# Performance work log

Hardware: AMD Instinct MI355X
Metric: run time of the kernel (lower is better)

Reference implementation:

```python
import jax, jax.numpy as jnp
import numpy as np

B, D_IN, D_OUT, DICT = 2048, 768, 768, 24576
TOP_K, TOP_K_AUX = 32, 512
L1_COEFF, AUX_PENALTY, N_DEAD = 0.001, 0.03125, 100.0


def setup_inputs() -> dict:
    key = jax.random.key(0)
    k1, k2, k3, k4, k5, k6 = jax.random.split(key, 6)
    x_in = jax.random.normal(k1, (B, D_IN), dtype=jnp.float32)
    y_target = jax.random.normal(k2, (B, D_OUT), dtype=jnp.float32)
    nb = jax.random.randint(k3, (DICT,), 0, 200).astype(jnp.float32)
    # kaiming-uniform-ish init
    bound_e = float(np.sqrt(6.0 / D_IN))
    W_enc = jax.random.uniform(k4, (D_IN, DICT), minval=-bound_e, maxval=bound_e, dtype=jnp.float32)
    bound_d = float(np.sqrt(6.0 / DICT))
    W_dec = jax.random.uniform(k5, (DICT, D_OUT), minval=-bound_d, maxval=bound_d, dtype=jnp.float32)
    W_dec = W_dec / jnp.linalg.norm(W_dec, axis=-1, keepdims=True)  # unit-norm rows
    b_dec = jnp.zeros((D_OUT,), dtype=jnp.float32)
    return {"x_in": x_in, "y_target": y_target, "num_batches_not_active": nb,
            "W_enc": W_enc, "W_dec": W_dec, "b_dec": b_dec}


def _unit_norm(x):
    m = x.mean(axis=-1, keepdims=True)
    x = x - m
    s = jnp.std(x, axis=-1, keepdims=True, ddof=1)  # torch .std is unbiased
    return x / (s + 1e-5), m, s


def reference(x_in, y_target, num_batches_not_active, W_enc, W_dec, b_dec):
    xn, _, _ = _unit_norm(x_in)
    yn, y_mean, y_std = _unit_norm(y_target)
    x_enc = xn - b_dec  # pre_enc_bias (input_size == output_size)
    acts = jax.nn.relu(x_enc @ W_enc)                      # [B, DICT]
    vals, idx = jax.lax.top_k(acts, TOP_K)                 # [B, TOP_K]
    rows = jnp.arange(B)[:, None]
    acts_sparse = jnp.zeros_like(acts).at[rows, idx].set(vals)
    y_pred = acts_sparse @ W_dec + b_dec                   # [B, D_OUT]
    y_pred_out = y_pred * y_std + y_mean

    # stateful dead-feature bookkeeping (update_inactive_features)
    col_active = acts_sparse.sum(axis=0) > 0
    nb = jnp.where(col_active, 0.0, num_batches_not_active + 1.0)

    l2_loss = jnp.mean((y_pred - yn) ** 2)
    l1_norm = jnp.mean(jnp.abs(acts_sparse).sum(axis=-1))
    l1_loss = L1_COEFF * l1_norm
    l0_norm = jnp.mean((acts_sparse > 0).astype(jnp.float32).sum(axis=-1))

    # auxiliary loss on dead features (static-shape masked top-k; masked cols
    # get -1 < relu acts so extras relu-clip to 0 -> same math as torch gather)
    dead = nb >= N_DEAD
    masked = jnp.where(dead[None, :], acts, -1.0)
    av, ai = jax.lax.top_k(masked, TOP_K_AUX)
    av = jax.nn.relu(av)
    acts_aux = jnp.zeros_like(acts).at[rows, ai].set(av)
    y_pred_aux = acts_aux @ W_dec
    residual = yn - y_pred
    l2_aux = AUX_PENALTY * jnp.mean((y_pred_aux - residual) ** 2)
    aux_loss = jnp.where(dead.any(), l2_aux, 0.0)

    loss = l2_loss + l1_loss + aux_loss
    num_dead_features = (nb > N_DEAD).sum()
    return (y_pred_out, acts_sparse, loss, l2_loss, l1_loss, l0_norm, l1_norm,
            aux_loss, num_dead_features)
```

## Files before the change

### kernel.cpp

```cpp
#include <hip/hip_runtime.h>
#include <math.h>

#define BATCH 2048
#define DIN 768
#define DICT 24576
#define KM 32
#define KA 512
#define NPT 48
#define L1_COEFF 0.001f
#define AUX_PENALTY 0.03125f
#define CAND_MAX 128
#define CAND_DELTA 0.08f
#define AUX_SPLIT 8
#define SAUX 18432
#define AGB ((DIN/128)*(BATCH/128)*AUX_SPLIT)

typedef __attribute__((ext_vector_type(8))) short bf16x8;
typedef __attribute__((ext_vector_type(8))) unsigned short u16x8;
typedef __attribute__((ext_vector_type(4))) float f32x4;

constexpr size_t WS_XENC   = 0;
constexpr size_t WS_YN     = WS_XENC + (size_t)BATCH*DIN;
constexpr size_t WS_YMEAN  = WS_YN + (size_t)BATCH*DIN;
constexpr size_t WS_YSTD   = WS_YMEAN + BATCH;
constexpr size_t WS_RES    = WS_YSTD + BATCH;
constexpr size_t WS_NSEL   = WS_RES + (size_t)BATCH*DIN;
constexpr size_t WS_SEL    = WS_NSEL + BATCH;
constexpr size_t WS_SELV   = WS_SEL + (size_t)BATCH*KM;
constexpr size_t WS_COLACT = WS_SELV + (size_t)BATCH*KM;
constexpr size_t WS_ACC    = WS_COLACT + DICT;
constexpr size_t WS_DB     = WS_ACC + 8;
constexpr size_t WS_XEB    = WS_DB + DICT/32;
constexpr size_t WS_WETF   = WS_XEB + (size_t)BATCH*DIN/2;
constexpr size_t WS_WETB   = WS_WETF + (size_t)DICT*DIN;
constexpr size_t WS_WDB    = WS_WETB + (size_t)DICT*DIN/2;
constexpr size_t WS_DPREF  = WS_XEB + DICT/32;
constexpr size_t WS_META   = WS_XEB + 2*(DICT/32);

__device__ __forceinline__ unsigned short f2b(float f){
    unsigned u = __float_as_uint(f);
    return (unsigned short)((u + 0x7fffu + ((u >> 16) & 1u)) >> 16);
}
__device__ __forceinline__ float b2f(unsigned short h){ return __uint_as_float(((unsigned)h) << 16); }

__device__ __forceinline__ void gld_lds16(const void* g, void* l){
    __builtin_amdgcn_global_load_lds(
        (const __attribute__((address_space(1))) unsigned int*)g,
        (__attribute__((address_space(3))) unsigned int*)l, 16, 0, 0);
}

__device__ __forceinline__ int blk_count512_w(int cw, int* s16, int par){
    if ((threadIdx.x & 63) == 0) s16[par*8 + (threadIdx.x >> 6)] = cw;
    __syncthreads();
    int tot = 0;
    #pragma unroll
    for (int w=0; w<8; w++) tot += s16[par*8+w];
    return tot;
}
__device__ __forceinline__ float blk_sum512(float v, float* s16, int par){
    #pragma unroll
    for (int off=32; off; off>>=1) v += __shfl_down(v, off);
    if ((threadIdx.x & 63) == 0) s16[par*8 + (threadIdx.x >> 6)] = v;
    __syncthreads();
    float t = 0.f;
    #pragma unroll
    for (int w=0; w<8; w++) t += s16[par*8+w];
    return t;
}
__device__ __forceinline__ float blk_sum256(float v, float* s8, int par){
    #pragma unroll
    for (int off=32; off; off>>=1) v += __shfl_down(v, off);
    if ((threadIdx.x & 63) == 0) s8[par*4 + (threadIdx.x >> 6)] = v;
    __syncthreads();
    float t = 0.f;
    #pragma unroll
    for (int w=0; w<4; w++) t += s8[par*4+w];
    return t;
}

__global__ __launch_bounds__(256) void prep_k(const float* __restrict__ x,
        const float* __restrict__ y, const float* __restrict__ bdec,
        const float* __restrict__ We, const float* __restrict__ Wd,
        float* __restrict__ Tf, unsigned short* __restrict__ Tb,
        unsigned short* __restrict__ Td, float* __restrict__ ws){
    __shared__ float s8[8];
    __shared__ float t1[32][33];
    __shared__ float t2[32][33];
    const int tid = threadIdx.x;
    if (blockIdx.x < 2*BATCH){
        int b = blockIdx.x; bool isy = b >= BATCH; int row = isy ? b - BATCH : b;
        if (b < 8){
            float* dst = ws + WS_COLACT;
            for (int i = b*256 + tid; i < DICT + 8; i += 2048) dst[i] = 0.f;
        }
        const float* src = (isy ? y : x) + (size_t)row*DIN;
        float v0 = src[tid], v1 = src[tid+256], v2 = src[tid+512];
        float s = blk_sum256(v0+v1+v2, s8, 0);
        float mean = s * (1.f/(float)DIN);
        float d0 = v0-mean, d1 = v1-mean, d2 = v2-mean;
        float vs = blk_sum256(d0*d0+d1*d1+d2*d2, s8, 1);
        float sd = sqrtf(vs / (float)(DIN-1));
        float inv = 1.f / (sd + 1e-5f);
        if (isy){
            float* yn = ws + WS_YN + (size_t)row*DIN;
            yn[tid] = d0*inv; yn[tid+256] = d1*inv; yn[tid+512] = d2*inv;
            if (tid==0){ ws[WS_YMEAN+row] = mean; ws[WS_YSTD+row] = sd; }
        } else {
            float* xe = ws + WS_XENC + (size_t)row*DIN;
            unsigned short* xeb = (unsigned short*)(ws + WS_XEB) + (size_t)row*DIN;
            float e0 = d0*inv - bdec[tid];
            float e1 = d1*inv - bdec[tid+256];
            float e2 = d2*inv - bdec[tid+512];
            xe[tid] = e0; xe[tid+256] = e1; xe[tid+512] = e2;
            xeb[tid] = f2b(e0); xeb[tid+256] = f2b(e1); xeb[tid+512] = f2b(e2);
        }
    } else {
        int t = blockIdx.x - 2*BATCH;
        int bx = t % (DICT/32), by = t / (DICT/32);
        int a0 = bx*32, k0 = by*32;
        int r = tid >> 5, c = tid & 31;
        #pragma unroll
        for (int rr=r; rr<32; rr+=8){
            t1[rr][c] = We[(size_t)(k0+rr)*DICT + a0 + c];
            t2[rr][c] = Wd[(size_t)(a0+rr)*DIN + k0 + c];
        }
        __syncthreads();
        #pragma unroll
        for (int rr=r; rr<32; rr+=8){
            float v = t1[c][rr];
            Tf[(size_t)(a0+rr)*DIN + k0 + c] = v;
            Tb[(size_t)(a0+rr)*DIN + k0 + c] = f2b(v);
            Td[(size_t)(k0+rr)*DICT + a0 + c] = f2b(t2[c][rr]);
        }
    }
}

__global__ __launch_bounds__(256) void gemm_mfma(const unsigned short* __restrict__ Abf,
        const unsigned short* __restrict__ Bbf, unsigned short* __restrict__ C){
    __shared__ __align__(16) unsigned short As[128*64];
    __shared__ __align__(16) unsigned short Bs[128*64];
    const int tid = threadIdx.x;
    const int w = tid >> 6, lane = tid & 63;
    const int g = blockIdx.x;
    const int xcd = g & 7;
    const int s_ = g >> 3;
    const int m_t = s_ & 15;
    const int n_t = xcd + 8*(s_ >> 4);
    const int m0 = m_t*128, n0 = n_t*128;
    const int srow = lane >> 3;
    const int schunk = (lane & 7) ^ srow;
    const int wm = (w >> 1)*64, wn = (w & 1)*64;
    f32x4 acc[16];
    #pragma unroll
    for (int i=0;i<16;i++) acc[i] = (f32x4){0.f,0.f,0.f,0.f};
    for (int kt = 0; kt < DIN; kt += 64){
        #pragma unroll
        for (int q=0;q<4;q++){
            int s = w*4 + q;
            int row = 8*s + srow;
            gld_lds16(Abf + (size_t)(m0+row)*DIN + kt + schunk*8, &As[8*s*64]);
            gld_lds16(Bbf + (size_t)(n0+row)*DIN + kt + schunk*8, &Bs[8*s*64]);
        }
        __syncthreads();
        #pragma unroll
        for (int kk=0; kk<64; kk+=32){
            bf16x8 af[4], bfr[4];
            int ch = (kk>>3) + (lane>>4);
            #pragma unroll
            for (int i=0;i<4;i++){
                int row = wm + i*16 + (lane&15);
                af[i] = *(const bf16x8*)&As[row*64 + ((ch ^ (row&7))<<3)];
            }
            #pragma unroll
            for (int j=0;j<4;j++){
                int row = wn + j*16 + (lane&15);
                bfr[j] = *(const bf16x8*)&Bs[row*64 + ((ch ^ (row&7))<<3)];
            }
            #pragma unroll
            for (int i=0;i<4;i++)
                #pragma unroll
                for (int j=0;j<4;j++)
                    acc[i*4+j] = __builtin_amdgcn_mfma_f32_16x16x32_bf16(af[i], bfr[j], acc[i*4+j], 0,0,0);
        }
        __syncthreads();
    }
    #pragma unroll
    for (int i=0;i<4;i++){
        #pragma unroll
        for (int r=0;r<4;r++){
            int m = m0 + wm + i*16 + (lane>>4)*4 + r;
            unsigned short* crow = C + (size_t)m*DICT + n0 + wn + (lane&15);
            #pragma unroll
            for (int j=0;j<4;j++)
                crow[j*16] = f2b(fmaxf(acc[i*4+j][r], 0.f) + 0.0f);
        }
    }
}

__global__ __launch_bounds__(512) void topk_main(const unsigned short* __restrict__ actsb,
        const float* __restrict__ WeTf, const float* __restrict__ Wdec,
        const float* __restrict__ bdec, float* __restrict__ ws,
        float* __restrict__ ypred_out){
    const int row = blockIdx.x, tid = threadIdx.x;
    const int lane = tid & 63, wid = tid >> 6;
    __shared__ int   s_i16[16];
    __shared__ float s_f16[16];
    __shared__ float s_x[DIN];
    __shared__ int   s_ci[CAND_MAX];
    __shared__ float s_cv[CAND_MAX];
    __shared__ int   s_li[KM];
    __shared__ float s_lv[KM];
    __shared__ int   s_n, s_m;
    const unsigned short* arow = actsb + (size_t)row * DICT;
    const float* xrow = ws + WS_XENC + (size_t)row * DIN;
    unsigned short h[NPT];
    #pragma unroll
    for (int i=0;i<6;i++){
        u16x8 v = *(const u16x8*)&arow[i*4096 + tid*8];
        #pragma unroll
        for (int e=0;e<8;e++) h[i*8+e] = v[e];
    }
    s_x[tid] = xrow[tid];
    if (tid < DIN-512) s_x[tid+512] = xrow[tid+512];
    if (tid == 0){ s_n = 0; s_m = 0; }

    int par = 0;
    unsigned prefix = 0;
    for (int bit=14; bit>=0; bit--){
        unsigned cand = prefix | (1u<<bit);
        int c = 0;
        #pragma unroll
        for (int q=0;q<NPT;q++) c += (int)__popcll(__ballot((unsigned)h[q] >= cand));
        int tot = blk_count512_w(c, s_i16, par); par ^= 1;
        if (tot >= KM) prefix = cand;
    }
    float tc = b2f((unsigned short)prefix) - CAND_DELTA;
    #pragma unroll
    for (int q=0;q<NPT;q++){
        if (b2f(h[q]) > tc){
            int p = atomicAdd(&s_n, 1);
            if (p < CAND_MAX) s_ci[p] = (q>>3)*4096 + tid*8 + (q&7);
        }
    }
    __syncthreads();
    int nc = s_n; if (nc > CAND_MAX) nc = CAND_MAX;
    for (int c = wid; c < nc; c += 8){
        const float* wr = WeTf + (size_t)s_ci[c]*DIN;
        float p = 0.f;
        #pragma unroll
        for (int t=0; t<12; t++) p = fmaf(s_x[lane + 64*t], wr[lane + 64*t], p);
        #pragma unroll
        for (int off=32; off; off>>=1) p += __shfl_down(p, off);
        if (lane == 0) s_cv[c] = fmaxf(p, 0.f);
    }
    __syncthreads();
    if (tid < nc){
        float vi = s_cv[tid]; int ii = s_ci[tid];
        int rank = 0;
        for (int j=0; j<nc; j++){
            float vj = s_cv[j];
            rank += (vj > vi) || (vj == vi && s_ci[j] < ii);
        }
        if (rank < KM){
            int p = atomicAdd(&s_m, 1);
            s_li[p] = ii; s_lv[p] = vi;
        }
    }
    __syncthreads();
    if (tid < KM){
        ((int*)ws)[WS_COLACT + s_li[tid]] = 1;
        ((int*)ws)[WS_SEL  + (size_t)row*KM + tid] = s_li[tid];
        ws[WS_SELV + (size_t)row*KM + tid] = s_lv[tid];
    }
    if (tid == 0){
        float l1 = 0.f; int l0 = 0;
        for (int l=0;l<KM;l++){ l1 += s_lv[l]; l0 += (s_lv[l] > 0.f); }
        atomicAdd(&ws[WS_ACC+1], l1);
        atomicAdd(&ws[WS_ACC+2], (float)l0);
    }
    __syncthreads();
    float ym = ws[WS_YMEAN+row], ys = ws[WS_YSTD+row];
    float l2loc = 0.f;
    for (int c = tid; c < DIN; c += 512){
        float acc = bdec[c];
        #pragma unroll 4
        for (int l=0;l<KM;l++) acc = fmaf(s_lv[l], Wdec[(size_t)s_li[l]*DIN + c], acc);
        float ynv = ws[WS_YN + (size_t)row*DIN + c];
        float d = acc - ynv;
        l2loc += d*d;
        ws[WS_RES + (size_t)row*DIN + c] = ynv - acc;
        ypred_out[(size_t)row*DIN + c] = fmaf(acc, ys, ym);
    }
    float l2t = blk_sum512(l2loc, s_f16, 0);
    if (tid==0) atomicAdd(&ws[WS_ACC+0], l2t);
}

__global__ __launch_bounds__(768) void deadscan_k(const float* __restrict__ nb,
        float* __restrict__ ws){
    __shared__ int s[DICT/32];
    __shared__ int c12[12];
    const int t = threadIdx.x;
    const int* colact = (const int*)ws + WS_COLACT;
    unsigned bits = 0; int cgt = 0;
    const int base = t*32;
    #pragma unroll 8
    for (int b=0;b<32;b++){
        int j = base + b;
        float nbn = colact[j] ? 0.f : nb[j] + 1.f;
        bits |= (nbn >= 100.f ? 1u : 0u) << b;
        cgt  += (nbn > 100.f) ? 1 : 0;
    }
    ((unsigned*)(ws + WS_DB))[t] = bits;
    int pc = __popc(bits);
    s[t] = pc;
    #pragma unroll
    for (int off=32; off; off>>=1) cgt += __shfl_down(cgt, off);
    if ((t & 63) == 0) c12[t >> 6] = cgt;
    __syncthreads();
    for (int off=1; off<DICT/32; off<<=1){
        int v = (t >= off) ? s[t-off] : 0;
        __syncthreads();
        s[t] += v;
        __syncthreads();
    }
    ((int*)(ws + WS_DPREF))[t] = s[t] - pc;
    if (t == DICT/32 - 1){
        int nd = s[t];
        int ndpad = (nd + 63) & ~63;
        if (ndpad > SAUX) ndpad = SAUX;
        int* meta = (int*)(ws + WS_META);
        meta[0] = nd; meta[1] = ndpad; meta[2] = ndpad >> 6;
        meta[3] = ((ndpad >> 6) + AUX_SPLIT - 1) / AUX_SPLIT;
        int tot = 0;
        #pragma unroll
        for (int wv=0; wv<12; wv++) tot += c12[wv];
        ws[WS_ACC+4] = (float)tot;
        ((int*)ws)[WS_ACC+5] = (nd > 0) ? 1 : 0;
    }
}

__global__ __launch_bounds__(512) void auxprep_k(const unsigned short* __restrict__ actsb,
        unsigned short* __restrict__ wdt, unsigned short* __restrict__ auxc,
        float* __restrict__ ws){
    __shared__ unsigned s_db[DICT/32];
    __shared__ int      s_dp[DICT/32];
    __shared__ int      s_i16[16];
    __shared__ unsigned short s_out[SAUX];
    const int tid = threadIdx.x;
    for (int i=tid; i<DICT/32; i+=512){
        s_db[i] = ((const unsigned*)(ws + WS_DB))[i];
        s_dp[i] = ((const int*)(ws + WS_DPREF))[i];
    }
    const int nd    = ((const int*)(ws + WS_META))[0];
    const int ndpad = ((const int*)(ws + WS_META))[1];
    __syncthreads();
    if (blockIdx.x < DIN){
        const int n = blockIdx.x;
        unsigned short* row = wdt + (size_t)n*DICT;
        #pragma unroll
        for (int i=0;i<6;i++){
            u16x8 a = *(const u16x8*)&row[i*4096 + tid*8];
            int w = i*128 + (tid>>2);
            unsigned dbw = s_db[w]; int dpw = s_dp[w];
            #pragma unroll
            for (int e=0;e<8;e++){
                int bit = (tid&3)*8 + e;
                if ((dbw >> bit) & 1u){
                    int p = dpw + __popc(dbw & ((1u<<bit)-1u));
                    if (p < SAUX) s_out[p] = a[e];
                }
            }
        }
        for (int t2 = nd + tid; t2 < ndpad; t2 += 512) s_out[t2] = 0;
        __syncthreads();
        for (int i = tid*8; i < ndpad; i += 4096)
            *(u16x8*)&row[i] = *(const u16x8*)&s_out[i];
    } else {
        const int row = blockIdx.x - DIN;
        const unsigned short* arow = actsb + (size_t)row * DICT;
        unsigned short key[NPT];
        #pragma unroll
        for (int i=0;i<6;i++){
            u16x8 v = *(const u16x8*)&arow[i*4096 + tid*8];
            unsigned dbw = s_db[i*128 + (tid>>2)];
            #pragma unroll
            for (int e=0;e<8;e++){
                unsigned short hv = v[e];
                key[i*8+e] = (((dbw >> ((tid&3)*8 + e)) & 1u) && hv) ? hv : 0;
            }
        }
        int par = 0;
        unsigned prefix = 0;
        for (int bit=14; bit>=0; bit--){
            unsigned cand = prefix | (1u<<bit);
            int c = 0;
            #pragma unroll
            for (int q=0;q<NPT;q++) c += (int)__popcll(__ballot((unsigned)key[q] >= cand));
            int tot = blk_count512_w(c, s_i16, par); par ^= 1;
            if (tot >= KA) prefix = cand;
        }
        unsigned thr = prefix ? prefix : 1u;
        #pragma unroll
        for (int i=0;i<6;i++){
            int w = i*128 + (tid>>2);
            unsigned dbw = s_db[w];
            int dpw = s_dp[w];
            #pragma unroll
            for (int e=0;e<8;e++){
                int bit = (tid&3)*8 + e;
                if ((dbw >> bit) & 1u){
                    int p = dpw + __popc(dbw & ((1u<<bit)-1u));
                    unsigned short kv = key[i*8+e];
                    if (p < SAUX) s_out[p] = ((unsigned)kv >= thr) ? kv : (unsigned short)0;
                }
            }
        }
        for (int t2 = nd + tid; t2 < ndpad; t2 += 512) s_out[t2] = 0;
        __syncthreads();
        unsigned short* crow = auxc + (size_t)row * SAUX;
        for (int i = tid*8; i < ndpad; i += 4096)
            *(u16x8*)&crow[i] = *(const u16x8*)&s_out[i];
    }
}

__global__ __launch_bounds__(256) void auxgz_k(const unsigned short* __restrict__ Abf,
        const unsigned short* __restrict__ Bbf, float* __restrict__ ws,
        float* __restrict__ acts){
    __shared__ __align__(16) unsigned short As[128*64];
    __shared__ __align__(16) unsigned short Bs[128*64];
    const int tid = threadIdx.x;
    if (blockIdx.x >= AGB){
        const int row = blockIdx.x - AGB;
        float4 z = make_float4(0.f,0.f,0.f,0.f);
        float4* arow4 = (float4*)(acts + (size_t)row*DICT);
        #pragma unroll
        for (int i=0;i<24;i++) arow4[tid + 256*i] = z;
        __syncthreads();
        if (tid < KM){
            int j   = ((const int*)ws)[WS_SEL + (size_t)row*KM + tid];
            float v = ws[WS_SELV + (size_t)row*KM + tid];
            (acts + (size_t)row*DICT)[j] = v;
        }
        return;
    }
    const int nkt   = ((const int*)(ws + WS_META))[2];
    const int chunk = ((const int*)(ws + WS_META))[3];
    const int g = blockIdx.x;
    const int z = g & 7;
    const int s_ = g >> 3;
    const int m_t = s_ & 15;
    const int n_t = s_ >> 4;
    int t0 = z * chunk;
    int t1 = t0 + chunk; if (t1 > nkt) t1 = nkt;
    const int w = tid >> 6, lane = tid & 63;
    const int m0 = m_t*128, n0 = n_t*128;
    const int srow = lane >> 3;
    const int schunk = (lane & 7) ^ srow;
    const int wm = (w >> 1)*64, wn = (w & 1)*64;
    f32x4 acc[16];
    #pragma unroll
    for (int i=0;i<16;i++) acc[i] = (f32x4){0.f,0.f,0.f,0.f};
    for (int t = t0; t < t1; ++t){
        int kt = t*64;
        #pragma unroll
        for (int q=0;q<4;q++){
            int s = w*4 + q;
            int row = 8*s + srow;
            gld_lds16(Abf + (size_t)(m0+row)*SAUX + kt + schunk*8, &As[8*s*64]);
            gld_lds16(Bbf + (size_t)(n0+row)*DICT + kt + schunk*8, &Bs[8*s*64]);
        }
        __syncthreads();
        #pragma unroll
        for (int kk=0; kk<64; kk+=32){
            bf16x8 af[4], bfr[4];
            int ch = (kk>>3) + (lane>>4);
            #pragma unroll
            for (int i=0;i<4;i++){
                int row = wm + i*16 + (lane&15);
                af[i] = *(const bf16x8*)&As[row*64 + ((ch ^ (row&7))<<3)];
            }
            #pragma unroll
            for (int j=0;j<4;j++){
                int row = wn + j*16 + (lane&15);
                bfr[j] = *(const bf16x8*)&Bs[row*64 + ((ch ^ (row&7))<<3)];
            }
            #pragma unroll
            for (int i=0;i<4;i++)
                #pragma unroll
                for (int j=0;j<4;j++)
                    acc[i*4+j] = __builtin_amdgcn_mfma_f32_16x16x32_bf16(af[i], bfr[j], acc[i*4+j], 0,0,0);
        }
        __syncthreads();
    }
    float* buf = ws + ((z < 6) ? (WS_WETB + (size_t)z*BATCH*DIN)
                               : (z == 6 ? WS_YN : WS_XENC));
    #pragma unroll
    for (int i=0;i<4;i++){
        #pragma unroll
        for (int r=0;r<4;r++){
            int m = m0 + wm + i*16 + (lane>>4)*4 + r;
            float* crow = buf + (size_t)m*DIN + n0 + wn + (lane&15);
            #pragma unroll
            for (int j=0;j<4;j++) crow[j*16] = acc[i*4+j][r];
        }
    }
}

__global__ __launch_bounds__(256) void auxloss_k(float* __restrict__ ws){
    __shared__ float s8[8];
    const float4* b0 = (const float4*)(ws + WS_WETB);
    const float4* b1 = (const float4*)(ws + WS_WETB + 1*(size_t)BATCH*DIN);
    const float4* b2 = (const float4*)(ws + WS_WETB + 2*(size_t)BATCH*DIN);
    const float4* b3 = (const float4*)(ws + WS_WETB + 3*(size_t)BATCH*DIN);
    const float4* b4 = (const float4*)(ws + WS_WETB + 4*(size_t)BATCH*DIN);
    const float4* b5 = (const float4*)(ws + WS_WETB + 5*(size_t)BATCH*DIN);
    const float4* b6 = (const float4*)(ws + WS_YN);
    const float4* b7 = (const float4*)(ws + WS_XENC);
    const float4* r4 = (const float4*)(ws + WS_RES);
    float s = 0.f;
    const size_t n4 = (size_t)BATCH*DIN/4;
    for (size_t i = (size_t)blockIdx.x*256 + threadIdx.x; i < n4; i += (size_t)gridDim.x*256){
        float4 a0 = b0[i], a1 = b1[i], a2 = b2[i], a3 = b3[i];
        float4 a4 = b4[i], a5 = b5[i], a6 = b6[i], a7 = b7[i];
        float4 rr = r4[i];
        float x0 = ((a0.x+a1.x)+(a2.x+a3.x))+((a4.x+a5.x)+(a6.x+a7.x)) - rr.x;
        float x1 = ((a0.y+a1.y)+(a2.y+a3.y))+((a4.y+a5.y)+(a6.y+a7.y)) - rr.y;
        float x2 = ((a0.z+a1.z)+(a2.z+a3.z))+((a4.z+a5.z)+(a6.z+a7.z)) - rr.z;
        float x3 = ((a0.w+a1.w)+(a2.w+a3.w))+((a4.w+a5.w)+(a6.w+a7.w)) - rr.w;
        s += x0*x0 + x1*x1 + x2*x2 + x3*x3;
    }
    float tot = blk_sum256(s, s8, 0);
    if (threadIdx.x == 0) atomicAdd(&ws[WS_ACC+3], tot);
}

__global__ void finalize_k(const float* __restrict__ ws, float* __restrict__ out){
    if (threadIdx.x == 0){
        float l2   = ws[WS_ACC+0] / (float)((size_t)BATCH*DIN);
        float l1n  = ws[WS_ACC+1] / (float)BATCH;
        float l1l  = L1_COEFF * l1n;
        float l0   = ws[WS_ACC+2] / (float)BATCH;
        float auxm = AUX_PENALTY * (ws[WS_ACC+3] / (float)((size_t)BATCH*DIN));
        int any    = ((const int*)ws)[WS_ACC+5];
        float auxl = any ? auxm : 0.f;
        out[0] = l2 + l1l + auxl;
        out[1] = l2;
        out[2] = l1l;
        out[3] = l0;
        out[4] = l1n;
        out[5] = auxl;
        out[6] = ws[WS_ACC+4];
    }
}

extern "C" void kernel_launch(void* const* d_in, const int* in_sizes, int n_in,
                              void* d_out, int out_size, void* d_ws, size_t ws_size,
                              hipStream_t stream){
    const float* x_in = (const float*)d_in[0];
    const float* y_t  = (const float*)d_in[1];
    const float* nb   = (const float*)d_in[2];
    const float* Wenc = (const float*)d_in[3];
    const float* Wdec = (const float*)d_in[4];
    const float* bdec = (const float*)d_in[5];
    float* out  = (float*)d_out;
    float* ws   = (float*)d_ws;
    float* acts = out + (size_t)BATCH*DIN;
    float* scal = out + (size_t)BATCH*DIN + (size_t)BATCH*DICT;
    unsigned short* actsb = (unsigned short*)acts;

    unsigned short* xeb  = (unsigned short*)(ws + WS_XEB);
    float*          wetf = ws + WS_WETF;
    unsigned short* wetb = (unsigned short*)(ws + WS_WETB);
    unsigned short* wdt  = (unsigned short*)(ws + WS_WDB);
    unsigned short* auxc = (unsigned short*)(ws + WS_WETF);

    prep_k<<<2*BATCH + (DICT/32)*(DIN/32), 256, 0, stream>>>(
        x_in, y_t, bdec, Wenc, Wdec, wetf, wetb, wdt, ws);
    gemm_mfma<<<(DICT/128)*(BATCH/128), 256, 0, stream>>>(xeb, wetb, actsb);
    topk_main<<<BATCH, 512, 0, stream>>>(actsb, wetf, Wdec, bdec, ws, out);
    deadscan_k<<<1, DICT/32, 0, stream>>>(nb, ws);
    auxprep_k<<<DIN + BATCH, 512, 0, stream>>>(actsb, wdt, auxc, ws);
    auxgz_k<<<AGB + BATCH, 256, 0, stream>>>(auxc, wdt, ws, acts);
    auxloss_k<<<256, 256, 0, stream>>>(ws);
    finalize_k<<<1, 64, 0, stream>>>(ws, scal);
}
```

Measured before the change: 840.9 us.

## Enlarge encoder GEMM tiles to 256x256 with double-buffered LDS pipelining

```diff
diff --git a/kernel.cpp b/kernel.cpp
--- a/kernel.cpp
+++ b/kernel.cpp
@@ -135,64 +135,137 @@
     }
 }
 
-__global__ __launch_bounds__(256) void gemm_mfma(const unsigned short* __restrict__ Abf,
+__global__ __launch_bounds__(512, 2) void gemm_mfma(const unsigned short* __restrict__ Abf,
         const unsigned short* __restrict__ Bbf, unsigned short* __restrict__ C){
-    __shared__ __align__(16) unsigned short As[128*64];
-    __shared__ __align__(16) unsigned short Bs[128*64];
+    __shared__ __align__(16) unsigned short As2[2][16384];
+    __shared__ __align__(16) unsigned short Bs2[2][16384];
     const int tid = threadIdx.x;
     const int w = tid >> 6, lane = tid & 63;
+    const int wr = w >> 2, wc = w & 3;
     const int g = blockIdx.x;
     const int xcd = g & 7;
     const int s_ = g >> 3;
-    const int m_t = s_ & 15;
-    const int n_t = xcd + 8*(s_ >> 4);
-    const int m0 = m_t*128, n0 = n_t*128;
+    const int m_t = s_ & 7;
+    const int n_t = xcd + 8*(s_ >> 3);
+    const int m0 = m_t*256, n0 = n_t*256;
     const int srow = lane >> 3;
     const int schunk = (lane & 7) ^ srow;
-    const int wm = (w >> 1)*64, wn = (w & 1)*64;
-    f32x4 acc[16];
-    #pragma unroll
-    for (int i=0;i<16;i++) acc[i] = (f32x4){0.f,0.f,0.f,0.f};
-    for (int kt = 0; kt < DIN; kt += 64){
-        #pragma unroll
-        for (int q=0;q<4;q++){
-            int s = w*4 + q;
-            int row = 8*s + srow;
-            gld_lds16(Abf + (size_t)(m0+row)*DIN + kt + schunk*8, &As[8*s*64]);
-            gld_lds16(Bbf + (size_t)(n0+row)*DIN + kt + schunk*8, &Bs[8*s*64]);
-        }
-        __syncthreads();
-        #pragma unroll
-        for (int kk=0; kk<64; kk+=32){
-            bf16x8 af[4], bfr[4];
-            int ch = (kk>>3) + (lane>>4);
+    const int l15 = lane & 15, l4 = lane >> 4;
+
+    f32x4 acc[8][4];
+    #pragma unroll
+    for (int i=0;i<8;i++)
+        #pragma unroll
+        for (int j=0;j<4;j++) acc[i][j] = (f32x4){0.f,0.f,0.f,0.f};
+
+    #define STAGE_Q(b,kt,q) { \
+        int sa = w*4 + (q); \
+        gld_lds16(Abf + (size_t)(m0 + 8*sa + srow)*DIN + (kt) + schunk*8, &As2[b][8*sa*64]); \
+        gld_lds16(Bbf + (size_t)(n0 + 8*sa + srow)*DIN + (kt) + schunk*8, &Bs2[b][8*sa*64]); }
+
+    #pragma unroll
+    for (int q=0;q<4;q++) STAGE_Q(0, 0, q);
+    asm volatile("s_waitcnt vmcnt(0)" ::: "memory");
+    __builtin_amdgcn_s_barrier();
+
+    for (int t = 0; t < 12; ++t){
+        const int cur = t & 1, nb = cur ^ 1;
+        const unsigned short* Ac = As2[cur];
+        const unsigned short* Bc = Bs2[cur];
+        const int ktn = (t+1)*64;
+        const bool more = t < 11;
+        bf16x8 af[4], bfr[4];
+        if (more) STAGE_Q(nb, ktn, 0);
+        {
+            int ch = l4;
+            #pragma unroll
+            for (int j=0;j<4;j++){
+                int row = wc*64 + j*16 + l15;
+                bfr[j] = *(const bf16x8*)&Bc[row*64 + ((ch ^ (row&7))<<3)];
+            }
             #pragma unroll
             for (int i=0;i<4;i++){
-                int row = wm + i*16 + (lane&15);
-                af[i] = *(const bf16x8*)&As[row*64 + ((ch ^ (row&7))<<3)];
-            }
+                int row = wr*128 + i*16 + l15;
+                af[i] = *(const bf16x8*)&Ac[row*64 + ((ch ^ (row&7))<<3)];
+            }
+        }
+        __builtin_amdgcn_s_barrier();
+        __builtin_amdgcn_s_setprio(1);
+        #pragma unroll
+        for (int i=0;i<4;i++)
+            #pragma unroll
+            for (int j=0;j<4;j++)
+                acc[i][j] = __builtin_amdgcn_mfma_f32_16x16x32_bf16(af[i], bfr[j], acc[i][j], 0,0,0);
+        __builtin_amdgcn_s_setprio(0);
+        if (more) STAGE_Q(nb, ktn, 1);
+        {
+            int ch = l4;
+            #pragma unroll
+            for (int i=0;i<4;i++){
+                int row = wr*128 + (i+4)*16 + l15;
+                af[i] = *(const bf16x8*)&Ac[row*64 + ((ch ^ (row&7))<<3)];
+            }
+        }
+        __builtin_amdgcn_s_barrier();
+        __builtin_amdgcn_s_setprio(1);
+        #pragma unroll
+        for (int i=0;i<4;i++)
+            #pragma unroll
+            for (int j=0;j<4;j++)
+                acc[i+4][j] = __builtin_amdgcn_mfma_f32_16x16x32_bf16(af[i], bfr[j], acc[i+4][j], 0,0,0);
+        __builtin_amdgcn_s_setprio(0);
+        if (more) STAGE_Q(nb, ktn, 2);
+        {
+            int ch = 4 + l4;
             #pragma unroll
             for (int j=0;j<4;j++){
-                int row = wn + j*16 + (lane&15);
-                bfr[j] = *(const bf16x8*)&Bs[row*64 + ((ch ^ (row&7))<<3)];
-            }
-            #pragma unroll
-            for (int i=0;i<4;i++)
-                #pragma unroll
-                for (int j=0;j<4;j++)
-                    acc[i*4+j] = __builtin_amdgcn_mfma_f32_16x16x32_bf16(af[i], bfr[j], acc[i*4+j], 0,0,0);
-        }
-        __syncthreads();
-    }
-    #pragma unroll
-    for (int i=0;i<4;i++){
+                int row = wc*64 + j*16 + l15;
+                bfr[j] = *(const bf16x8*)&Bc[row*64 + ((ch ^ (row&7))<<3)];
+            }
+            #pragma unroll
+            for (int i=0;i<4;i++){
+                int row = wr*128 + i*16 + l15;
+                af[i] = *(const bf16x8*)&Ac[row*64 + ((ch ^ (row&7))<<3)];
+            }
+        }
+        __builtin_amdgcn_s_barrier();
+        __builtin_amdgcn_s_setprio(1);
+        #pragma unroll
+        for (int i=0;i<4;i++)
+            #pragma unroll
+            for (int j=0;j<4;j++)
+                acc[i][j] = __builtin_amdgcn_mfma_f32_16x16x32_bf16(af[i], bfr[j], acc[i][j], 0,0,0);
+        __builtin_amdgcn_s_setprio(0);
+        if (more) STAGE_Q(nb, ktn, 3);
+        {
+            int ch = 4 + l4;
+            #pragma unroll
+            for (int i=0;i<4;i++){
+                int row = wr*128 + (i+4)*16 + l15;
+                af[i] = *(const bf16x8*)&Ac[row*64 + ((ch ^ (row&7))<<3)];
+            }
+        }
+        __builtin_amdgcn_s_barrier();
+        __builtin_amdgcn_s_setprio(1);
+        #pragma unroll
+        for (int i=0;i<4;i++)
+            #pragma unroll
+            for (int j=0;j<4;j++)
+                acc[i+4][j] = __builtin_amdgcn_mfma_f32_16x16x32_bf16(af[i], bfr[j], acc[i+4][j], 0,0,0);
+        __builtin_amdgcn_s_setprio(0);
+        asm volatile("s_waitcnt vmcnt(0)" ::: "memory");
+        __builtin_amdgcn_s_barrier();
+    }
+    #undef STAGE_Q
+    #pragma unroll
+    for (int i=0;i<8;i++){
         #pragma unroll
         for (int r=0;r<4;r++){
-            int m = m0 + wm + i*16 + (lane>>4)*4 + r;
-            unsigned short* crow = C + (size_t)m*DICT + n0 + wn + (lane&15);
+            int m = m0 + wr*128 + i*16 + l4*4 + r;
+            unsigned short* crow = C + (size_t)m*DICT + n0 + wc*64 + l15;
             #pragma unroll
             for (int j=0;j<4;j++)
-                crow[j*16] = f2b(fmaxf(acc[i*4+j][r], 0.f) + 0.0f);
+                crow[j*16] = f2b(fmaxf(acc[i][j][r], 0.f) + 0.0f);
         }
     }
 }
@@ -575,7 +648,7 @@
 
     prep_k<<<2*BATCH + (DICT/32)*(DIN/32), 256, 0, stream>>>(
         x_in, y_t, bdec, Wenc, Wdec, wetf, wetb, wdt, ws);
-    gemm_mfma<<<(DICT/128)*(BATCH/128), 256, 0, stream>>>(xeb, wetb, actsb);
+    gemm_mfma<<<(DICT/256)*(BATCH/256), 512, 0, stream>>>(xeb, wetb, actsb);
     topk_main<<<BATCH, 512, 0, stream>>>(actsb, wetf, Wdec, bdec, ws, out);
     deadscan_k<<<1, DICT/32, 0, stream>>>(nb, ws);
     auxprep_k<<<DIN + BATCH, 512, 0, stream>>>(actsb, wdt, auxc, ws);
```

After: 844.4 us. Within noise of the previous version (+0.4%).
